# Kernel tuning notes

Measured on AMD Instinct MI355X. Metric: run time of the kernel, lower is better.

## Reference

```python
import math
import jax, jax.numpy as jnp
import numpy as np

EMB_DIM, EMB_KS, EMB_HS = 64, 2, 1
H, CS = 4, 32  # n_heads, GLA chunk size
EPS = 1e-5


def _ln4d(x, g, b):
    # LayerNormalization4D: normalize over channel dim (axis 1), biased var
    mu = x.mean(1, keepdims=True)
    var = ((x - mu) ** 2).mean(1, keepdims=True)
    return (x - mu) / jnp.sqrt(var + EPS) * g + b


def _unfold(x):
    # x [N,C,Q] -> [N, L, C*ks]; torch F.unfold feature order is c-major, k-minor
    N, C, Q = x.shape
    L = (Q - EMB_KS) // EMB_HS + 1
    f = jnp.stack([x[:, :, k:k + L] for k in range(EMB_KS)], axis=2)  # [N,C,ks,L]
    return f.reshape(N, C * EMB_KS, L).transpose(0, 2, 1)


def _deconv1d(x, w, b):
    # ConvTranspose1d, stride=EMB_HS=1; x [N,Cin,L], w [Cin,Cout,K]
    N, Cin, L = x.shape
    Cout, K = w.shape[1], w.shape[2]
    out_len = (L - 1) * EMB_HS + K
    y = jnp.zeros((N, Cout, out_len), x.dtype)
    for k in range(K):
        y = y.at[:, :, k:k + L].add(jnp.einsum('ncl,co->nol', x, w[:, :, k]))
    return y + b[None, :, None]


def _gla(x, Wq, Wk, Wv, Wg1, Wg2, Wr, gn, Wo):
    # chunked gated linear attention (use_gk=True, use_gv=False, swish output gate)
    N, L, D = x.shape
    Dk = Wq.shape[1] // H
    Dv = Wv.shape[1] // H
    Lp = -(-L // CS) * CS
    pad = Lp - L
    nc = Lp // CS
    q = (x @ Wq) * (Dk ** -0.5)
    k = x @ Wk
    v = x @ Wv
    gk = jax.nn.log_sigmoid((x @ Wg1) @ Wg2) / 32.0  # gate_logit_normalizer=32

    def chunk(t, dh):
        t = jnp.pad(t, ((0, 0), (0, pad), (0, 0)))
        return t.reshape(N, nc, CS, H, dh)

    q, k, gk, v = chunk(q, Dk), chunk(k, Dk), chunk(gk, Dk), chunk(v, Dv)
    gc = jnp.cumsum(gk, axis=2)                      # within-chunk log-decay [N,nc,CS,H,Dk]
    q_i = q * jnp.exp(gc)
    k_i = k * jnp.exp(-gc)
    mask = jnp.tril(jnp.ones((CS, CS), bool))
    A = jnp.einsum('ncthd,ncshd->nchts', q_i, k_i)   # intra-chunk scores
    A = jnp.where(mask[None, None, None], A, 0.0)
    o_intra = jnp.einsum('nchts,ncshd->ncthd', A, v)
    gl = gc[:, :, -1]                                 # chunk-total log decay [N,nc,H,Dk]
    k_o = k * jnp.exp(gl[:, :, None] - gc)

    def step(S, inp):
        qi, ko, vc, g = inp
        o = jnp.einsum('nthk,nhkv->nthv', qi, S)      # inter-chunk contribution
        S = S * jnp.exp(g)[..., None] + jnp.einsum('nthk,nthv->nhkv', ko, vc)
        return S, o

    S0 = jnp.zeros((N, H, Dk, Dv), x.dtype)
    xs = tuple(jnp.moveaxis(t, 1, 0) for t in (q_i, k_o, v, gl))
    _, o_inter = jax.lax.scan(step, S0, xs)
    o = (o_intra + jnp.moveaxis(o_inter, 0, 1)).reshape(N, Lp, H, Dv)[:, :L]
    # per-head RMSNorm + swish output gate
    o = o / jnp.sqrt(jnp.mean(o * o, -1, keepdims=True) + EPS) * gn.reshape(H, Dv)
    r = x @ Wr
    o = o.reshape(N, L, H * Dv) * (r * jax.nn.sigmoid(r))
    return o @ Wo


def _forward(x, mouth, intra_gamma, intra_beta, intra_Wq, intra_Wk, intra_Wv,
             intra_Wg1, intra_Wg2, intra_Wr, intra_gn, intra_Wo, intra_ct_w, intra_ct_b,
             inter_gamma, inter_beta, inter_Wq, inter_Wk, inter_Wv,
             inter_Wg1, inter_Wg2, inter_Wr, inter_gn, inter_Wo, inter_ct_w, inter_ct_b):
    B, C, old_T, old_Q = x.shape
    T = math.ceil((old_T - EMB_KS) / EMB_HS) * EMB_HS + EMB_KS
    Q = math.ceil((old_Q - EMB_KS) / EMB_HS) * EMB_HS + EMB_KS
    x = jnp.pad(x, ((0, 0), (0, 0), (0, T - old_T), (0, Q - old_Q)))
    # intra (frequency) path
    u = _ln4d(x, intra_gamma, intra_beta)
    u = u.transpose(0, 2, 1, 3).reshape(B * T, C, Q)
    f = _unfold(u)                                    # [B*T, Q-1, C*ks]
    g = _gla(f, intra_Wq, intra_Wk, intra_Wv, intra_Wg1, intra_Wg2, intra_Wr, intra_gn, intra_Wo)
    y = _deconv1d(g.transpose(0, 2, 1), intra_ct_w, intra_ct_b)  # [B*T, C, Q]
    y = y.reshape(B, T, C, Q).transpose(0, 2, 1, 3) + x
    # inter (time) path
    u = _ln4d(y, inter_gamma, inter_beta)
    u = u.transpose(0, 3, 1, 2).reshape(B * Q, C, T)
    f = _unfold(u)                                    # [B*Q, T-1, C*ks]
    g = _gla(f, inter_Wq, inter_Wk, inter_Wv, inter_Wg1, inter_Wg2, inter_Wr, inter_gn, inter_Wo)
    z = _deconv1d(g.transpose(0, 2, 1), inter_ct_w, inter_ct_b)  # [B*Q, C, T]
    z = z.reshape(B, Q, C, T).transpose(0, 2, 3, 1) + y
    return z[..., :old_T, :old_Q]


def setup_inputs() -> dict:
    key = jax.random.key(0)
    ks = jax.random.split(key, 32)
    D = EMB_DIM * EMB_KS       # 128 = GLA d_model
    DKV = 2 * D                # 256 (expand_k = expand_v = 2)

    def w(i, shape, fan):
        return jax.random.normal(ks[i], shape, jnp.float32) / np.sqrt(fan).astype(np.float32)

    inp = {
        'x': jax.random.normal(ks[0], (4, EMB_DIM, 256, 128), jnp.float32),
        'mouth': jax.random.normal(ks[1], (4, 1, 64, 64), jnp.float32),
    }
    for p, base in (('intra', 2), ('inter', 14)):
        inp[p + '_gamma'] = jnp.ones((1, EMB_DIM, 1, 1), jnp.float32)
        inp[p + '_beta'] = jnp.zeros((1, EMB_DIM, 1, 1), jnp.float32)
        inp[p + '_Wq'] = w(base, (D, DKV), D)
        inp[p + '_Wk'] = w(base + 1, (D, DKV), D)
        inp[p + '_Wv'] = w(base + 2, (D, DKV), D)
        inp[p + '_Wg1'] = w(base + 3, (D, 32), D)
        inp[p + '_Wg2'] = w(base + 4, (32, DKV), 32)
        inp[p + '_Wr'] = w(base + 5, (D, DKV), D)
        inp[p + '_gn'] = jnp.ones((DKV,), jnp.float32)
        inp[p + '_Wo'] = w(base + 6, (DKV, D), DKV)
        inp[p + '_ct_w'] = w(base + 7, (D, EMB_DIM, EMB_KS), D * EMB_KS)
        inp[p + '_ct_b'] = jnp.zeros((EMB_DIM,), jnp.float32)
    return inp


def reference(x, mouth, intra_gamma, intra_beta, intra_Wq, intra_Wk, intra_Wv,
              intra_Wg1, intra_Wg2, intra_Wr, intra_gn, intra_Wo, intra_ct_w, intra_ct_b,
              inter_gamma, inter_beta, inter_Wq, inter_Wk, inter_Wv,
              inter_Wg1, inter_Wg2, inter_Wr, inter_gn, inter_Wo, inter_ct_w, inter_ct_b):
    return _forward(x, mouth, intra_gamma, intra_beta, intra_Wq, intra_Wk, intra_Wv,
                    intra_Wg1, intra_Wg2, intra_Wr, intra_gn, intra_Wo, intra_ct_w, intra_ct_b,
                    inter_gamma, inter_beta, inter_Wq, inter_Wk, inter_Wv,
                    inter_Wg1, inter_Wg2, inter_Wr, inter_gn, inter_Wo, inter_ct_w, inter_ct_b)
```

## Files before the change

kernel.cpp:

```cpp
#include <hip/hip_runtime.h>

#define EPS 1e-5f

__device__ __forceinline__ float logsig(float z) {
    return fminf(z, 0.0f) - log1pf(__expf(-fabsf(z)));
}

template<int SLEN, int PSTRIDE>
__global__ __launch_bounds__(512)
__attribute__((amdgpu_waves_per_eu(2, 2)))
void gla_pass(const float* __restrict__ src, float* __restrict__ out,
              const float* __restrict__ gamma, const float* __restrict__ beta,
              const float* __restrict__ Wq, const float* __restrict__ Wk,
              const float* __restrict__ Wv, const float* __restrict__ Wg1,
              const float* __restrict__ Wg2, const float* __restrict__ Wr,
              const float* __restrict__ gn, const float* __restrict__ Wo,
              const float* __restrict__ ctw, const float* __restrict__ ctb)
{
    constexpr int NC = SLEN / 32;
    constexpr int L  = SLEN - 1;

    __shared__ __align__(16) float sxA[64][36];
    __shared__ __align__(16) float sxB[64][36];
    __shared__ __align__(16) float sxr[64][32];
    __shared__ __align__(16) float qf[32][256];
    __shared__ __align__(16) float kf[32][256];
    __shared__ __align__(16) float voc[32][256];
    __shared__ __align__(16) float uni[4608];
    __shared__ __align__(16) float fw1t[32][36];
    __shared__ __align__(16) float gprevs[128];
    __shared__ float egl[256];
    __shared__ float sgam[64], sbet[64];
    __shared__ float smu[33], sinv[33];
    __shared__ float gcarry[256];

    float* const Ats  = uni;
    float* const gdec = uni;

    const int tid  = threadIdx.x;
    const int lane = tid & 63;
    const int wv   = tid >> 6;
    const int h    = wv & 3;
    const int kh   = wv >> 2;
    const int d    = tid & 255;
    const int th   = (tid >> 8) & 1;
    const int n    = blockIdx.x;

    int b, fixedoff;
    if constexpr (PSTRIDE == 1) { b = n >> 8; fixedoff = (n & 255) * 128; }
    else                        { b = n >> 7; fixedoff = (n & 127); }
    const int cbase = (b * 64) * 32768 + fixedoff;

    if (tid < 64)  { sgam[tid] = gamma[tid]; sbet[tid] = beta[tid]; }
    if (tid < 128) gprevs[tid] = 0.0f;

    float S[32];
    #pragma unroll
    for (int k = 0; k < 32; ++k) S[k] = 0.0f;

    const float gnv  = gn[h * 64 + lane];
    const float bias = ctb[lane];

    #pragma unroll
    for (int k = 0; k < 5; ++k) {
        int idx = tid + k * 512;
        if (idx < 64 * 33) {
            int cc = idx / 33, i = idx - cc * 33;
            sxA[cc][i] = src[cbase + cc * 32768 + i * PSTRIDE];
        }
    }

    for (int ch = 0; ch < NC; ++ch) {
        const int l0 = ch * 32;
        float (* const cur)[36] = (ch & 1) ? sxB : sxA;
        float (* const nxt)[36] = (ch & 1) ? sxA : sxB;
        __syncthreads();

        float pre[5];
        const bool pf = (ch + 1 < NC);
        if (pf) {
            const int l0n = l0 + 32;
            #pragma unroll
            for (int k = 0; k < 5; ++k) {
                int idx = tid + k * 512;
                if (idx < 64 * 33) {
                    int cc = idx / 33, i = idx - cc * 33;
                    int p  = l0n + i; if (p > SLEN - 1) p = SLEN - 1;
                    pre[k] = src[cbase + cc * 32768 + p * PSTRIDE];
                }
            }
        }

        for (int col = wv; col < 33; col += 8) {
            float x = cur[lane][col];
            float s1 = x, s2 = x * x;
            #pragma unroll
            for (int off = 32; off > 0; off >>= 1) {
                s1 += __shfl_xor(s1, off, 64);
                s2 += __shfl_xor(s2, off, 64);
            }
            if (lane == 0) {
                float mu  = s1 * (1.0f / 64.0f);
                float var = s2 * (1.0f / 64.0f) - mu * mu;
                smu[col]  = mu;
                sinv[col] = rsqrtf(fmaxf(var, 0.0f) + EPS);
            }
        }
        __syncthreads();

        #pragma unroll
        for (int k = 0; k < 5; ++k) {
            int idx = tid + k * 512;
            if (idx < 64 * 33) {
                int cc = idx / 33, i = idx - cc * 33;
                float x = cur[cc][i];
                if (i < 32) sxr[cc][i] = x;
                cur[cc][i] = (x - smu[i]) * sinv[i] * sgam[cc] + sbet[cc];
            }
        }
        __syncthreads();

        {
            const int m = tid & 31, tg2 = tid >> 5;
            float a0 = 0.0f, a1 = 0.0f;
            #pragma unroll 2
            for (int cc = 0; cc < 64; ++cc) {
                const float w0 = Wg1[(2*cc)*32 + m], w1 = Wg1[(2*cc+1)*32 + m];
                a0 += cur[cc][tg2]      * w0 + cur[cc][tg2 + 1]  * w1;
                a1 += cur[cc][tg2 + 16] * w0 + cur[cc][tg2 + 17] * w1;
            }
            fw1t[m][tg2] = a0; fw1t[m][tg2 + 16] = a1;
        }
        __syncthreads();

        float rn[16];
        {
            const int t0 = th * 16;
            float acc2[16];
            #pragma unroll
            for (int t = 0; t < 16; ++t) acc2[t] = 0.0f;
            for (int mm = 0; mm < 32; ++mm) {
                const float w = Wg2[mm * 256 + d];
                #pragma unroll
                for (int i = 0; i < 4; ++i) {
                    float4 f4 = *(const float4*)&fw1t[mm][t0 + 4 * i];
                    acc2[4*i+0] += f4.x * w; acc2[4*i+1] += f4.y * w;
                    acc2[4*i+2] += f4.z * w; acc2[4*i+3] += f4.w * w;
                }
            }
            float r = 0.0f;
            #pragma unroll
            for (int t = 0; t < 16; ++t) {
                if ((l0 + t0 + t) < L) r += logsig(acc2[t]) * (1.0f / 32.0f);
                acc2[t] = r;
            }
            if (th == 0) gcarry[d] = r;
            __syncthreads();
            const float c = (th == 0) ? 0.0f : gcarry[d];
            #pragma unroll
            for (int t = 0; t < 16; ++t) rn[t] = c + acc2[t];
            if (th == 1) egl[d] = __expf(rn[15]);
        }

        if (pf) {
            #pragma unroll
            for (int k = 0; k < 5; ++k) {
                int idx = tid + k * 512;
                if (idx < 64 * 33) {
                    int cc = idx / 33, i = idx - cc * 33;
                    nxt[cc][i] = pre[k];
                }
            }
        }

        {
            const int t0 = th * 16;
            float aq[16], ak[16];
            #pragma unroll
            for (int t = 0; t < 16; ++t) { aq[t] = 0.0f; ak[t] = 0.0f; }
            for (int cc = 0; cc < 64; ++cc) {
                float col[17];
                #pragma unroll
                for (int i = 0; i < 4; ++i) {
                    float4 c4 = *(const float4*)&cur[cc][t0 + 4 * i];
                    col[4*i] = c4.x; col[4*i+1] = c4.y; col[4*i+2] = c4.z; col[4*i+3] = c4.w;
                }
                col[16] = cur[cc][t0 + 16];
                const float wq0 = Wq[(2*cc)*256 + d], wq1 = Wq[(2*cc+1)*256 + d];
                const float wk0 = Wk[(2*cc)*256 + d], wk1 = Wk[(2*cc+1)*256 + d];
                #pragma unroll
                for (int t = 0; t < 16; ++t) {
                    aq[t] += col[t] * wq0 + col[t+1] * wq1;
                    ak[t] += col[t] * wk0 + col[t+1] * wk1;
                }
            }
            #pragma unroll
            for (int t = 0; t < 16; ++t) {
                bool valid = (l0 + t0 + t) < L;
                qf[t0 + t][d] = valid ? aq[t] * 0.125f * __expf(rn[t]) : 0.0f;
                kf[t0 + t][d] = valid ? ak[t] * __expf(-rn[t]) : 0.0f;
            }
        }
        float ar[16];
        {
            const int t0 = th * 16;
            float av[16];
            #pragma unroll
            for (int t = 0; t < 16; ++t) { av[t] = 0.0f; ar[t] = 0.0f; }
            #pragma unroll 2
            for (int cc = 0; cc < 64; ++cc) {
                float col[17];
                #pragma unroll
                for (int i = 0; i < 4; ++i) {
                    float4 c4 = *(const float4*)&cur[cc][t0 + 4 * i];
                    col[4*i] = c4.x; col[4*i+1] = c4.y; col[4*i+2] = c4.z; col[4*i+3] = c4.w;
                }
                col[16] = cur[cc][t0 + 16];
                const float wv0 = Wv[(2*cc)*256 + d], wv1 = Wv[(2*cc+1)*256 + d];
                const float wr0 = Wr[(2*cc)*256 + d], wr1 = Wr[(2*cc+1)*256 + d];
                #pragma unroll
                for (int t = 0; t < 16; ++t) {
                    av[t] += col[t] * wv0 + col[t+1] * wv1;
                    ar[t] += col[t] * wr0 + col[t+1] * wr1;
                }
            }
            #pragma unroll
            for (int t = 0; t < 16; ++t)
                voc[t0 + t][d] = ((l0 + t0 + t) < L) ? av[t] : 0.0f;
        }
        __syncthreads();

        const int base = h * 64;
        float vcol[32];
        #pragma unroll
        for (int t = 0; t < 32; ++t) vcol[t] = voc[t][base + lane];

        for (int pi = lane + 64 * kh; pi < 528; pi += 128) {
            float fpi = (float)pi;
            int t = (int)((sqrtf(8.0f * fpi + 1.0f) - 1.0f) * 0.5f);
            if (((t + 1) * (t + 2)) / 2 <= pi) ++t;
            if ((t * (t + 1)) / 2 > pi) --t;
            int s = pi - (t * (t + 1)) / 2;
            float a = 0.0f;
            #pragma unroll
            for (int ii = 0; ii < 16; ++ii) {
                int i = (ii + lane) & 15;
                float4 q4 = *(const float4*)&qf[t][base + 4 * i];
                float4 k4 = *(const float4*)&kf[s][base + 4 * i];
                a += q4.x*k4.x + q4.y*k4.y + q4.z*k4.z + q4.w*k4.w;
            }
            Ats[h * 1152 + t * 36 + s] = a;
        }
        __syncthreads();

        if (kh == 1) {
            #pragma unroll
            for (int t = 0; t < 32; ++t) {
                float oe = 0.0f;
                #pragma unroll
                for (int i = 0; i < 8; ++i) {
                    float4 q4 = *(const float4*)&qf[t][base + 32 + 4 * i];
                    oe += q4.x*S[4*i] + q4.y*S[4*i+1] + q4.z*S[4*i+2] + q4.w*S[4*i+3];
                }
                voc[t][base + lane] = oe;
            }
        }
        __syncthreads();

        if (kh == 0) {
            #pragma unroll
            for (int t = 0; t < 32; ++t) {
                float ot = voc[t][base + lane];
                #pragma unroll
                for (int i = 0; i < 8; ++i) {
                    float4 q4 = *(const float4*)&qf[t][base + 4 * i];
                    ot += q4.x*S[4*i] + q4.y*S[4*i+1] + q4.z*S[4*i+2] + q4.w*S[4*i+3];
                }
                const float* arow = &Ats[h * 1152 + t * 36];
                #pragma unroll
                for (int s4 = 0; s4 + 4 <= t + 1; s4 += 4) {
                    float4 a4 = *(const float4*)&arow[s4];
                    ot += a4.x*vcol[s4] + a4.y*vcol[s4+1] + a4.z*vcol[s4+2] + a4.w*vcol[s4+3];
                }
                #pragma unroll
                for (int s = (t + 1) & ~3; s <= t; ++s) ot += arow[s] * vcol[s];
                float ss = ot * ot;
                #pragma unroll
                for (int off = 32; off > 0; off >>= 1) ss += __shfl_xor(ss, off, 64);
                voc[t][base + lane] = ot * rsqrtf(ss * (1.0f / 64.0f) + EPS) * gnv;
            }
        } else {
            const int kb = base + 32;
            #pragma unroll
            for (int i = 0; i < 8; ++i) {
                float s0 = 0.0f, s1 = 0.0f, s2 = 0.0f, s3 = 0.0f;
                #pragma unroll
                for (int t = 0; t < 32; ++t) {
                    float4 k4 = *(const float4*)&kf[t][kb + 4 * i];
                    const float vt = vcol[t];
                    s0 += k4.x * vt; s1 += k4.y * vt; s2 += k4.z * vt; s3 += k4.w * vt;
                }
                S[4*i+0] = egl[kb + 4*i+0] * (S[4*i+0] + s0);
                S[4*i+1] = egl[kb + 4*i+1] * (S[4*i+1] + s1);
                S[4*i+2] = egl[kb + 4*i+2] * (S[4*i+2] + s2);
                S[4*i+3] = egl[kb + 4*i+3] * (S[4*i+3] + s3);
            }
        }
        __syncthreads();

        if (kh == 0) {
            const int kb = base;
            #pragma unroll
            for (int i = 0; i < 8; ++i) {
                float s0 = 0.0f, s1 = 0.0f, s2 = 0.0f, s3 = 0.0f;
                #pragma unroll
                for (int t = 0; t < 32; ++t) {
                    float4 k4 = *(const float4*)&kf[t][kb + 4 * i];
                    const float vt = vcol[t];
                    s0 += k4.x * vt; s1 += k4.y * vt; s2 += k4.z * vt; s3 += k4.w * vt;
                }
                S[4*i+0] = egl[kb + 4*i+0] * (S[4*i+0] + s0);
                S[4*i+1] = egl[kb + 4*i+1] * (S[4*i+1] + s1);
                S[4*i+2] = egl[kb + 4*i+2] * (S[4*i+2] + s2);
                S[4*i+3] = egl[kb + 4*i+3] * (S[4*i+3] + s3);
            }
        }

        {
            const int t0 = th * 16;
            #pragma unroll
            for (int t = 0; t < 16; ++t) {
                const float r = ar[t];
                voc[t0 + t][d] *= r / (1.0f + __expf(-r));
            }
        }
        __syncthreads();

        {
            const int m2  = tid & 63;
            const int tg4 = tid >> 6;
            float accA[4] = {0,0,0,0}, accB[4] = {0,0,0,0};
            for (int j = 0; j < 256; j += 4) {
                float wA0 = Wo[(j+0)*128 + m2],      wB0 = Wo[(j+0)*128 + m2 + 64];
                float wA1 = Wo[(j+1)*128 + m2],      wB1 = Wo[(j+1)*128 + m2 + 64];
                float wA2 = Wo[(j+2)*128 + m2],      wB2 = Wo[(j+2)*128 + m2 + 64];
                float wA3 = Wo[(j+3)*128 + m2],      wB3 = Wo[(j+3)*128 + m2 + 64];
                #pragma unroll
                for (int i = 0; i < 4; ++i) {
                    float4 o4 = *(const float4*)&voc[tg4 * 4 + i][j];
                    accA[i] += o4.x*wA0 + o4.y*wA1 + o4.z*wA2 + o4.w*wA3;
                    accB[i] += o4.x*wB0 + o4.y*wB1 + o4.z*wB2 + o4.w*wB3;
                }
            }
            #pragma unroll
            for (int i = 0; i < 4; ++i) {
                gdec[(tg4 * 4 + i) * 132 + m2]      = accA[i];
                gdec[(tg4 * 4 + i) * 132 + m2 + 64] = accB[i];
            }
        }
        __syncthreads();

        {
            const int o  = lane;
            const int pg = wv;
            const float2* ctw2 = (const float2*)ctw;
            float acc4[4] = {0,0,0,0};
            for (int c4 = 0; c4 < 128; c4 += 4) {
                float2 w0 = ctw2[(c4+0)*64 + o];
                float2 w1 = ctw2[(c4+1)*64 + o];
                float2 w2 = ctw2[(c4+2)*64 + o];
                float2 w3 = ctw2[(c4+3)*64 + o];
                float4 r[5];
                r[0] = (pg == 0) ? *(const float4*)&gprevs[c4]
                                 : *(const float4*)&gdec[(pg*4 - 1) * 132 + c4];
                #pragma unroll
                for (int j = 0; j < 4; ++j)
                    r[j+1] = *(const float4*)&gdec[(pg*4 + j) * 132 + c4];
                #pragma unroll
                for (int i = 0; i < 4; ++i) {
                    acc4[i] += r[i+1].x*w0.x + r[i].x*w0.y
                             + r[i+1].y*w1.x + r[i].y*w1.y
                             + r[i+1].z*w2.x + r[i].z*w2.y
                             + r[i+1].w*w3.x + r[i].w*w3.y;
                }
            }
            #pragma unroll
            for (int i = 0; i < 4; ++i) {
                const int tl = pg * 4 + i;
                const int oi = cbase + o * 32768 + (l0 + tl) * PSTRIDE;
                out[oi] = acc4[i] + bias + sxr[o][tl];
            }
        }
        __syncthreads();
        if (tid < 128) gprevs[tid] = gdec[31 * 132 + tid];
    }
}

extern "C" void kernel_launch(void* const* d_in, const int* in_sizes, int n_in,
                              void* d_out, int out_size, void* d_ws, size_t ws_size,
                              hipStream_t stream)
{
    const float* x = (const float*)d_in[0];
    float* y = (float*)d_ws;
    float* z = (float*)d_out;

    gla_pass<128, 1><<<dim3(1024), dim3(512), 0, stream>>>(
        x, y,
        (const float*)d_in[2],  (const float*)d_in[3],  (const float*)d_in[4],
        (const float*)d_in[5],  (const float*)d_in[6],  (const float*)d_in[7],
        (const float*)d_in[8],  (const float*)d_in[9],  (const float*)d_in[10],
        (const float*)d_in[11], (const float*)d_in[12], (const float*)d_in[13]);

    gla_pass<256, 128><<<dim3(512), dim3(512), 0, stream>>>(
        y, z,
        (const float*)d_in[14], (const float*)d_in[15], (const float*)d_in[16],
        (const float*)d_in[17], (const float*)d_in[18], (const float*)d_in[19],
        (const float*)d_in[20], (const float*)d_in[21], (const float*)d_in[22],
        (const float*)d_in[23], (const float*)d_in[24], (const float*)d_in[25]);
}
```

Measured before the change: 6.395 ms.

## Restructure GLA pass to 256-thread blocks with per-head single-wave state

```diff
diff --git a/kernel.cpp b/kernel.cpp
--- a/kernel.cpp
+++ b/kernel.cpp
@@ -7,8 +7,7 @@
 }
 
 template<int SLEN, int PSTRIDE>
-__global__ __launch_bounds__(512)
-__attribute__((amdgpu_waves_per_eu(2, 2)))
+__global__ __launch_bounds__(256, 2)
 void gla_pass(const float* __restrict__ src, float* __restrict__ out,
               const float* __restrict__ gamma, const float* __restrict__ beta,
               const float* __restrict__ Wq, const float* __restrict__ Wk,
@@ -20,30 +19,17 @@
     constexpr int NC = SLEN / 32;
     constexpr int L  = SLEN - 1;
 
-    __shared__ __align__(16) float sxA[64][36];
-    __shared__ __align__(16) float sxB[64][36];
-    __shared__ __align__(16) float sxr[64][32];
-    __shared__ __align__(16) float qf[32][256];
-    __shared__ __align__(16) float kf[32][256];
-    __shared__ __align__(16) float voc[32][256];
-    __shared__ __align__(16) float uni[4608];
-    __shared__ __align__(16) float fw1t[32][36];
-    __shared__ __align__(16) float gprevs[128];
+    __shared__ __align__(16) float sx[64][36];
+    __shared__ __align__(16) float qfR[32 * 260];
+    __shared__ __align__(16) float kfR[32 * 260];
     __shared__ float egl[256];
+    __shared__ float gprevs[128];
     __shared__ float sgam[64], sbet[64];
-    __shared__ float smu[33], sinv[33];
-    __shared__ float gcarry[256];
-
-    float* const Ats  = uni;
-    float* const gdec = uni;
 
     const int tid  = threadIdx.x;
     const int lane = tid & 63;
-    const int wv   = tid >> 6;
-    const int h    = wv & 3;
-    const int kh   = wv >> 2;
-    const int d    = tid & 255;
-    const int th   = (tid >> 8) & 1;
+    const int h    = tid >> 6;
+    const int base = h * 64;
     const int n    = blockIdx.x;
 
     int b, fixedoff;
@@ -54,45 +40,45 @@
     if (tid < 64)  { sgam[tid] = gamma[tid]; sbet[tid] = beta[tid]; }
     if (tid < 128) gprevs[tid] = 0.0f;
 
-    float S[32];
+    float S[64];
     #pragma unroll
-    for (int k = 0; k < 32; ++k) S[k] = 0.0f;
-
-    const float gnv  = gn[h * 64 + lane];
-    const float bias = ctb[lane];
+    for (int k = 0; k < 64; ++k) S[k] = 0.0f;
+
+    const float gnv  = gn[base + lane];
+    const int   oc   = tid & 63;
+    const int   pg   = tid >> 6;
+    const float bias = ctb[oc];
 
     #pragma unroll
-    for (int k = 0; k < 5; ++k) {
-        int idx = tid + k * 512;
-        if (idx < 64 * 33) {
+    for (int k = 0; k < 9; ++k) {
+        int idx = tid + k * 256;
+        if (idx < 2112) {
             int cc = idx / 33, i = idx - cc * 33;
-            sxA[cc][i] = src[cbase + cc * 32768 + i * PSTRIDE];
+            sx[cc][i] = src[cbase + cc * 32768 + i * PSTRIDE];
         }
     }
 
     for (int ch = 0; ch < NC; ++ch) {
         const int l0 = ch * 32;
-        float (* const cur)[36] = (ch & 1) ? sxB : sxA;
-        float (* const nxt)[36] = (ch & 1) ? sxA : sxB;
-        __syncthreads();
-
-        float pre[5];
+        __syncthreads();
+
+        float pre[9];
         const bool pf = (ch + 1 < NC);
         if (pf) {
-            const int l0n = l0 + 32;
-            #pragma unroll
-            for (int k = 0; k < 5; ++k) {
-                int idx = tid + k * 512;
-                if (idx < 64 * 33) {
+            #pragma unroll
+            for (int k = 0; k < 9; ++k) {
+                int idx = tid + k * 256;
+                if (idx < 2112) {
                     int cc = idx / 33, i = idx - cc * 33;
-                    int p  = l0n + i; if (p > SLEN - 1) p = SLEN - 1;
+                    int p = l0 + 32 + i; if (p > SLEN - 1) p = SLEN - 1;
                     pre[k] = src[cbase + cc * 32768 + p * PSTRIDE];
                 }
             }
         }
 
-        for (int col = wv; col < 33; col += 8) {
-            float x = cur[lane][col];
+        if (ch > 0 && tid < 128) gprevs[tid] = kfR[31 * 260 + tid];
+        for (int col = h; col < 33; col += 4) {
+            float x = sx[lane][col];
             float s1 = x, s2 = x * x;
             #pragma unroll
             for (int off = 32; off > 0; off >>= 1) {
@@ -102,297 +88,259 @@
             if (lane == 0) {
                 float mu  = s1 * (1.0f / 64.0f);
                 float var = s2 * (1.0f / 64.0f) - mu * mu;
-                smu[col]  = mu;
-                sinv[col] = rsqrtf(fmaxf(var, 0.0f) + EPS);
-            }
-        }
-        __syncthreads();
-
-        #pragma unroll
-        for (int k = 0; k < 5; ++k) {
-            int idx = tid + k * 512;
-            if (idx < 64 * 33) {
+                qfR[col]      = mu;
+                qfR[64 + col] = rsqrtf(fmaxf(var, 0.0f) + EPS);
+            }
+        }
+        __syncthreads();
+
+        #pragma unroll
+        for (int k = 0; k < 9; ++k) {
+            int idx = tid + k * 256;
+            if (idx < 2112) {
                 int cc = idx / 33, i = idx - cc * 33;
-                float x = cur[cc][i];
-                if (i < 32) sxr[cc][i] = x;
-                cur[cc][i] = (x - smu[i]) * sinv[i] * sgam[cc] + sbet[cc];
-            }
-        }
-        __syncthreads();
-
-        {
-            const int m = tid & 31, tg2 = tid >> 5;
-            float a0 = 0.0f, a1 = 0.0f;
-            #pragma unroll 2
+                sx[cc][i] = (sx[cc][i] - qfR[i]) * qfR[64 + i] * sgam[cc] + sbet[cc];
+            }
+        }
+        __syncthreads();
+
+        {
+            const int m = tid & 31, tg = tid >> 5;
+            float a0 = 0, a1 = 0, a2 = 0, a3 = 0;
             for (int cc = 0; cc < 64; ++cc) {
-                const float w0 = Wg1[(2*cc)*32 + m], w1 = Wg1[(2*cc+1)*32 + m];
-                a0 += cur[cc][tg2]      * w0 + cur[cc][tg2 + 1]  * w1;
-                a1 += cur[cc][tg2 + 16] * w0 + cur[cc][tg2 + 17] * w1;
-            }
-            fw1t[m][tg2] = a0; fw1t[m][tg2 + 16] = a1;
-        }
-        __syncthreads();
-
-        float rn[16];
-        {
-            const int t0 = th * 16;
-            float acc2[16];
-            #pragma unroll
-            for (int t = 0; t < 16; ++t) acc2[t] = 0.0f;
+                float w0 = Wg1[(2*cc)*32 + m], w1 = Wg1[(2*cc+1)*32 + m];
+                float4 c4 = *(const float4*)&sx[cc][tg * 4];
+                float  c1 = sx[cc][tg * 4 + 4];
+                a0 += c4.x*w0 + c4.y*w1;
+                a1 += c4.y*w0 + c4.z*w1;
+                a2 += c4.z*w0 + c4.w*w1;
+                a3 += c4.w*w0 + c1  *w1;
+            }
+            kfR[m*260 + tg*4 + 0] = a0;
+            kfR[m*260 + tg*4 + 1] = a1;
+            kfR[m*260 + tg*4 + 2] = a2;
+            kfR[m*260 + tg*4 + 3] = a3;
+        }
+        __syncthreads();
+
+        float rn[32];
+        {
+            float acc[32];
+            #pragma unroll
+            for (int t = 0; t < 32; ++t) acc[t] = 0.0f;
             for (int mm = 0; mm < 32; ++mm) {
-                const float w = Wg2[mm * 256 + d];
-                #pragma unroll
-                for (int i = 0; i < 4; ++i) {
-                    float4 f4 = *(const float4*)&fw1t[mm][t0 + 4 * i];
-                    acc2[4*i+0] += f4.x * w; acc2[4*i+1] += f4.y * w;
-                    acc2[4*i+2] += f4.z * w; acc2[4*i+3] += f4.w * w;
+                float w = Wg2[mm * 256 + tid];
+                #pragma unroll
+                for (int i = 0; i < 8; ++i) {
+                    float4 f4 = *(const float4*)&kfR[mm*260 + 4*i];
+                    acc[4*i+0] += f4.x * w; acc[4*i+1] += f4.y * w;
+                    acc[4*i+2] += f4.z * w; acc[4*i+3] += f4.w * w;
                 }
             }
             float r = 0.0f;
             #pragma unroll
-            for (int t = 0; t < 16; ++t) {
-                if ((l0 + t0 + t) < L) r += logsig(acc2[t]) * (1.0f / 32.0f);
-                acc2[t] = r;
-            }
-            if (th == 0) gcarry[d] = r;
-            __syncthreads();
-            const float c = (th == 0) ? 0.0f : gcarry[d];
-            #pragma unroll
-            for (int t = 0; t < 16; ++t) rn[t] = c + acc2[t];
-            if (th == 1) egl[d] = __expf(rn[15]);
-        }
+            for (int t = 0; t < 32; ++t) {
+                if (l0 + t < L) r += logsig(acc[t]) * (1.0f / 32.0f);
+                rn[t] = r;
+            }
+            egl[tid] = __expf(rn[31]);
+        }
+        __syncthreads();
+
+
+        {
+            float aq[32];
+            #pragma unroll
+            for (int t = 0; t < 32; ++t) aq[t] = 0.0f;
+            for (int cc = 0; cc < 64; ++cc) {
+                float w0 = Wq[(2*cc)*256 + tid], w1 = Wq[(2*cc+1)*256 + tid];
+                float col[33];
+                #pragma unroll
+                for (int i = 0; i < 8; ++i) {
+                    float4 c4 = *(const float4*)&sx[cc][4*i];
+                    col[4*i]=c4.x; col[4*i+1]=c4.y; col[4*i+2]=c4.z; col[4*i+3]=c4.w;
+                }
+                col[32] = sx[cc][32];
+                #pragma unroll
+                for (int t = 0; t < 32; ++t) aq[t] += col[t]*w0 + col[t+1]*w1;
+            }
+            #pragma unroll
+            for (int t = 0; t < 32; ++t)
+                qfR[t*260 + tid] = (l0 + t < L) ? aq[t] * 0.125f * __expf(rn[t]) : 0.0f;
+        }
+        {
+            float ak[32];
+            #pragma unroll
+            for (int t = 0; t < 32; ++t) ak[t] = 0.0f;
+            for (int cc = 0; cc < 64; ++cc) {
+                float w0 = Wk[(2*cc)*256 + tid], w1 = Wk[(2*cc+1)*256 + tid];
+                float col[33];
+                #pragma unroll
+                for (int i = 0; i < 8; ++i) {
+                    float4 c4 = *(const float4*)&sx[cc][4*i];
+                    col[4*i]=c4.x; col[4*i+1]=c4.y; col[4*i+2]=c4.z; col[4*i+3]=c4.w;
+                }
+                col[32] = sx[cc][32];
+                #pragma unroll
+                for (int t = 0; t < 32; ++t) ak[t] += col[t]*w0 + col[t+1]*w1;
+            }
+            #pragma unroll
+            for (int t = 0; t < 32; ++t)
+                kfR[t*260 + tid] = (l0 + t < L) ? ak[t] * __expf(-rn[t]) : 0.0f;
+        }
+        float av[32], ar[32];
+        {
+            #pragma unroll
+            for (int t = 0; t < 32; ++t) { av[t] = 0.0f; ar[t] = 0.0f; }
+            for (int cc = 0; cc < 64; ++cc) {
+                float wv0 = Wv[(2*cc)*256 + tid], wv1 = Wv[(2*cc+1)*256 + tid];
+                float wr0 = Wr[(2*cc)*256 + tid], wr1 = Wr[(2*cc+1)*256 + tid];
+                float col[33];
+                #pragma unroll
+                for (int i = 0; i < 8; ++i) {
+                    float4 c4 = *(const float4*)&sx[cc][4*i];
+                    col[4*i]=c4.x; col[4*i+1]=c4.y; col[4*i+2]=c4.z; col[4*i+3]=c4.w;
+                }
+                col[32] = sx[cc][32];
+                #pragma unroll
+                for (int t = 0; t < 32; ++t) {
+                    av[t] += col[t]*wv0 + col[t+1]*wv1;
+                    ar[t] += col[t]*wr0 + col[t+1]*wr1;
+                }
+            }
+            #pragma unroll
+            for (int t = 0; t < 32; ++t) if (l0 + t >= L) av[t] = 0.0f;
+        }
+
+        float a[9];
+        #pragma unroll
+        for (int j = 0; j < 9; ++j) a[j] = 0.0f;
+        #pragma unroll
+        for (int j = 0; j < 9; ++j) {
+            int pi = lane + 64 * j;
+            if (pi < 528) {
+                float fpi = (float)pi;
+                int t = (int)((sqrtf(8.0f * fpi + 1.0f) - 1.0f) * 0.5f);
+                if (((t + 1) * (t + 2)) / 2 <= pi) ++t;
+                if ((t * (t + 1)) / 2 > pi) --t;
+                int s = pi - (t * (t + 1)) / 2;
+                float acc = 0.0f;
+                #pragma unroll
+                for (int ii = 0; ii < 16; ++ii) {
+                    int i = (ii + lane) & 15;
+                    float4 q4 = *(const float4*)&qfR[t*260 + base + 4*i];
+                    float4 k4 = *(const float4*)&kfR[s*260 + base + 4*i];
+                    acc += q4.x*k4.x + q4.y*k4.y + q4.z*k4.z + q4.w*k4.w;
+                }
+                a[j] = acc;
+            }
+        }
+
+        #pragma unroll
+        for (int t = 0; t < 32; ++t) {
+            float ot = 0.0f;
+            #pragma unroll
+            for (int i = 0; i < 16; ++i) {
+                float4 q4 = *(const float4*)&qfR[t*260 + base + 4*i];
+                ot += q4.x*S[4*i] + q4.y*S[4*i+1] + q4.z*S[4*i+2] + q4.w*S[4*i+3];
+            }
+            #pragma unroll
+            for (int s = 0; s <= t; ++s) {
+                const int pi = (t * (t + 1)) / 2 + s;
+                ot += __shfl(a[pi >> 6], pi & 63, 64) * av[s];
+            }
+            float ss = ot * ot;
+            #pragma unroll
+            for (int off = 32; off > 0; off >>= 1) ss += __shfl_xor(ss, off, 64);
+            qfR[t*260 + base + lane] = ot * rsqrtf(ss * (1.0f / 64.0f) + EPS) * gnv;
+        }
+
+        #pragma unroll
+        for (int i = 0; i < 16; ++i) {
+            float s0 = 0, s1 = 0, s2 = 0, s3 = 0;
+            #pragma unroll
+            for (int t = 0; t < 32; ++t) {
+                float4 k4 = *(const float4*)&kfR[t*260 + base + 4*i];
+                float vt = av[t];
+                s0 += k4.x*vt; s1 += k4.y*vt; s2 += k4.z*vt; s3 += k4.w*vt;
+            }
+            S[4*i+0] = egl[base + 4*i+0] * (S[4*i+0] + s0);
+            S[4*i+1] = egl[base + 4*i+1] * (S[4*i+1] + s1);
+            S[4*i+2] = egl[base + 4*i+2] * (S[4*i+2] + s2);
+            S[4*i+3] = egl[base + 4*i+3] * (S[4*i+3] + s3);
+        }
+
+        #pragma unroll
+        for (int t = 0; t < 32; ++t) {
+            float r = ar[t];
+            qfR[t*260 + tid] *= r / (1.0f + __expf(-r));
+        }
+        __syncthreads();
 
         if (pf) {
             #pragma unroll
-            for (int k = 0; k < 5; ++k) {
-                int idx = tid + k * 512;
-                if (idx < 64 * 33) {
+            for (int k = 0; k < 9; ++k) {
+                int idx = tid + k * 256;
+                if (idx < 2112) {
                     int cc = idx / 33, i = idx - cc * 33;
-                    nxt[cc][i] = pre[k];
-                }
-            }
-        }
-
-        {
-            const int t0 = th * 16;
-            float aq[16], ak[16];
-            #pragma unroll
-            for (int t = 0; t < 16; ++t) { aq[t] = 0.0f; ak[t] = 0.0f; }
-            for (int cc = 0; cc < 64; ++cc) {
-                float col[17];
-                #pragma unroll
-                for (int i = 0; i < 4; ++i) {
-                    float4 c4 = *(const float4*)&cur[cc][t0 + 4 * i];
-                    col[4*i] = c4.x; col[4*i+1] = c4.y; col[4*i+2] = c4.z; col[4*i+3] = c4.w;
-                }
-                col[16] = cur[cc][t0 + 16];
-                const float wq0 = Wq[(2*cc)*256 + d], wq1 = Wq[(2*cc+1)*256 + d];
-                const float wk0 = Wk[(2*cc)*256 + d], wk1 = Wk[(2*cc+1)*256 + d];
-                #pragma unroll
-                for (int t = 0; t < 16; ++t) {
-                    aq[t] += col[t] * wq0 + col[t+1] * wq1;
-                    ak[t] += col[t] * wk0 + col[t+1] * wk1;
-                }
-            }
-            #pragma unroll
-            for (int t = 0; t < 16; ++t) {
-                bool valid = (l0 + t0 + t) < L;
-                qf[t0 + t][d] = valid ? aq[t] * 0.125f * __expf(rn[t]) : 0.0f;
-                kf[t0 + t][d] = valid ? ak[t] * __expf(-rn[t]) : 0.0f;
-            }
-        }
-        float ar[16];
-        {
-            const int t0 = th * 16;
-            float av[16];
-            #pragma unroll
-            for (int t = 0; t < 16; ++t) { av[t] = 0.0f; ar[t] = 0.0f; }
-            #pragma unroll 2
-            for (int cc = 0; cc < 64; ++cc) {
-                float col[17];
-                #pragma unroll
-                for (int i = 0; i < 4; ++i) {
-                    float4 c4 = *(const float4*)&cur[cc][t0 + 4 * i];
-                    col[4*i] = c4.x; col[4*i+1] = c4.y; col[4*i+2] = c4.z; col[4*i+3] = c4.w;
-                }
-                col[16] = cur[cc][t0 + 16];
-                const float wv0 = Wv[(2*cc)*256 + d], wv1 = Wv[(2*cc+1)*256 + d];
-                const float wr0 = Wr[(2*cc)*256 + d], wr1 = Wr[(2*cc+1)*256 + d];
-                #pragma unroll
-                for (int t = 0; t < 16; ++t) {
-                    av[t] += col[t] * wv0 + col[t+1] * wv1;
-                    ar[t] += col[t] * wr0 + col[t+1] * wr1;
-                }
-            }
-            #pragma unroll
-            for (int t = 0; t < 16; ++t)
-                voc[t0 + t][d] = ((l0 + t0 + t) < L) ? av[t] : 0.0f;
-        }
-        __syncthreads();
-
-        const int base = h * 64;
-        float vcol[32];
-        #pragma unroll
-        for (int t = 0; t < 32; ++t) vcol[t] = voc[t][base + lane];
-
-        for (int pi = lane + 64 * kh; pi < 528; pi += 128) {
-            float fpi = (float)pi;
-            int t = (int)((sqrtf(8.0f * fpi + 1.0f) - 1.0f) * 0.5f);
-            if (((t + 1) * (t + 2)) / 2 <= pi) ++t;
-            if ((t * (t + 1)) / 2 > pi) --t;
-            int s = pi - (t * (t + 1)) / 2;
-            float a = 0.0f;
-            #pragma unroll
-            for (int ii = 0; ii < 16; ++ii) {
-                int i = (ii + lane) & 15;
-                float4 q4 = *(const float4*)&qf[t][base + 4 * i];
-                float4 k4 = *(const float4*)&kf[s][base + 4 * i];
-                a += q4.x*k4.x + q4.y*k4.y + q4.z*k4.z + q4.w*k4.w;
-            }
-            Ats[h * 1152 + t * 36 + s] = a;
-        }
-        __syncthreads();
-
-        if (kh == 1) {
-            #pragma unroll
-            for (int t = 0; t < 32; ++t) {
-                float oe = 0.0f;
-                #pragma unroll
-                for (int i = 0; i < 8; ++i) {
-                    float4 q4 = *(const float4*)&qf[t][base + 32 + 4 * i];
-                    oe += q4.x*S[4*i] + q4.y*S[4*i+1] + q4.z*S[4*i+2] + q4.w*S[4*i+3];
-                }
-                voc[t][base + lane] = oe;
-            }
-        }
-        __syncthreads();
-
-        if (kh == 0) {
-            #pragma unroll
-            for (int t = 0; t < 32; ++t) {
-                float ot = voc[t][base + lane];
-                #pragma unroll
-                for (int i = 0; i < 8; ++i) {
-                    float4 q4 = *(const float4*)&qf[t][base + 4 * i];
-                    ot += q4.x*S[4*i] + q4.y*S[4*i+1] + q4.z*S[4*i+2] + q4.w*S[4*i+3];
-                }
-                const float* arow = &Ats[h * 1152 + t * 36];
-                #pragma unroll
-                for (int s4 = 0; s4 + 4 <= t + 1; s4 += 4) {
-                    float4 a4 = *(const float4*)&arow[s4];
-                    ot += a4.x*vcol[s4] + a4.y*vcol[s4+1] + a4.z*vcol[s4+2] + a4.w*vcol[s4+3];
-                }
-                #pragma unroll
-                for (int s = (t + 1) & ~3; s <= t; ++s) ot += arow[s] * vcol[s];
-                float ss = ot * ot;
-                #pragma unroll
-                for (int off = 32; off > 0; off >>= 1) ss += __shfl_xor(ss, off, 64);
-                voc[t][base + lane] = ot * rsqrtf(ss * (1.0f / 64.0f) + EPS) * gnv;
-            }
-        } else {
-            const int kb = base + 32;
-            #pragma unroll
-            for (int i = 0; i < 8; ++i) {
-                float s0 = 0.0f, s1 = 0.0f, s2 = 0.0f, s3 = 0.0f;
-                #pragma unroll
-                for (int t = 0; t < 32; ++t) {
-                    float4 k4 = *(const float4*)&kf[t][kb + 4 * i];
-                    const float vt = vcol[t];
-                    s0 += k4.x * vt; s1 += k4.y * vt; s2 += k4.z * vt; s3 += k4.w * vt;
-                }
-                S[4*i+0] = egl[kb + 4*i+0] * (S[4*i+0] + s0);
-                S[4*i+1] = egl[kb + 4*i+1] * (S[4*i+1] + s1);
-                S[4*i+2] = egl[kb + 4*i+2] * (S[4*i+2] + s2);
-                S[4*i+3] = egl[kb + 4*i+3] * (S[4*i+3] + s3);
-            }
-        }
-        __syncthreads();
-
-        if (kh == 0) {
-            const int kb = base;
-            #pragma unroll
-            for (int i = 0; i < 8; ++i) {
-                float s0 = 0.0f, s1 = 0.0f, s2 = 0.0f, s3 = 0.0f;
-                #pragma unroll
-                for (int t = 0; t < 32; ++t) {
-                    float4 k4 = *(const float4*)&kf[t][kb + 4 * i];
-                    const float vt = vcol[t];
-                    s0 += k4.x * vt; s1 += k4.y * vt; s2 += k4.z * vt; s3 += k4.w * vt;
-                }
-                S[4*i+0] = egl[kb + 4*i+0] * (S[4*i+0] + s0);
-                S[4*i+1] = egl[kb + 4*i+1] * (S[4*i+1] + s1);
-                S[4*i+2] = egl[kb + 4*i+2] * (S[4*i+2] + s2);
-                S[4*i+3] = egl[kb + 4*i+3] * (S[4*i+3] + s3);
-            }
-        }
-
-        {
-            const int t0 = th * 16;
-            #pragma unroll
-            for (int t = 0; t < 16; ++t) {
-                const float r = ar[t];
-                voc[t0 + t][d] *= r / (1.0f + __expf(-r));
-            }
-        }
-        __syncthreads();
-
-        {
-            const int m2  = tid & 63;
-            const int tg4 = tid >> 6;
-            float accA[4] = {0,0,0,0}, accB[4] = {0,0,0,0};
-            for (int j = 0; j < 256; j += 4) {
-                float wA0 = Wo[(j+0)*128 + m2],      wB0 = Wo[(j+0)*128 + m2 + 64];
-                float wA1 = Wo[(j+1)*128 + m2],      wB1 = Wo[(j+1)*128 + m2 + 64];
-                float wA2 = Wo[(j+2)*128 + m2],      wB2 = Wo[(j+2)*128 + m2 + 64];
-                float wA3 = Wo[(j+3)*128 + m2],      wB3 = Wo[(j+3)*128 + m2 + 64];
-                #pragma unroll
-                for (int i = 0; i < 4; ++i) {
-                    float4 o4 = *(const float4*)&voc[tg4 * 4 + i][j];
-                    accA[i] += o4.x*wA0 + o4.y*wA1 + o4.z*wA2 + o4.w*wA3;
-                    accB[i] += o4.x*wB0 + o4.y*wB1 + o4.z*wB2 + o4.w*wB3;
-                }
-            }
-            #pragma unroll
-            for (int i = 0; i < 4; ++i) {
-                gdec[(tg4 * 4 + i) * 132 + m2]      = accA[i];
-                gdec[(tg4 * 4 + i) * 132 + m2 + 64] = accB[i];
-            }
-        }
-        __syncthreads();
-
-        {
-            const int o  = lane;
-            const int pg = wv;
+                    sx[cc][i] = pre[k];
+                }
+            }
+        }
+        float resid[8];
+        #pragma unroll
+        for (int r2 = 0; r2 < 8; ++r2)
+            resid[r2] = src[cbase + oc * 32768 + (l0 + pg * 8 + r2) * PSTRIDE];
+
+        {
+            const int m2 = tid & 127, rh = tid >> 7;
+            float acc[16];
+            #pragma unroll
+            for (int r2 = 0; r2 < 16; ++r2) acc[r2] = 0.0f;
+            for (int jb = 0; jb < 64; ++jb) {
+                float w0 = Wo[(4*jb+0)*128 + m2];
+                float w1 = Wo[(4*jb+1)*128 + m2];
+                float w2 = Wo[(4*jb+2)*128 + m2];
+                float w3 = Wo[(4*jb+3)*128 + m2];
+                #pragma unroll
+                for (int r2 = 0; r2 < 16; ++r2) {
+                    float4 o4 = *(const float4*)&qfR[(rh*16 + r2)*260 + 4*jb];
+                    acc[r2] += o4.x*w0 + o4.y*w1 + o4.z*w2 + o4.w*w3;
+                }
+            }
+            #pragma unroll
+            for (int r2 = 0; r2 < 16; ++r2)
+                kfR[(rh*16 + r2)*260 + m2] = acc[r2];
+        }
+        __syncthreads();
+
+        {
             const float2* ctw2 = (const float2*)ctw;
-            float acc4[4] = {0,0,0,0};
+            float acc8[8];
+            #pragma unroll
+            for (int r2 = 0; r2 < 8; ++r2) acc8[r2] = 0.0f;
             for (int c4 = 0; c4 < 128; c4 += 4) {
-                float2 w0 = ctw2[(c4+0)*64 + o];
-                float2 w1 = ctw2[(c4+1)*64 + o];
-                float2 w2 = ctw2[(c4+2)*64 + o];
-                float2 w3 = ctw2[(c4+3)*64 + o];
-                float4 r[5];
-                r[0] = (pg == 0) ? *(const float4*)&gprevs[c4]
-                                 : *(const float4*)&gdec[(pg*4 - 1) * 132 + c4];
-                #pragma unroll
-                for (int j = 0; j < 4; ++j)
-                    r[j+1] = *(const float4*)&gdec[(pg*4 + j) * 132 + c4];
-                #pragma unroll
-                for (int i = 0; i < 4; ++i) {
-                    acc4[i] += r[i+1].x*w0.x + r[i].x*w0.y
-                             + r[i+1].y*w1.x + r[i].y*w1.y
-                             + r[i+1].z*w2.x + r[i].z*w2.y
-                             + r[i+1].w*w3.x + r[i].w*w3.y;
-                }
-            }
-            #pragma unroll
-            for (int i = 0; i < 4; ++i) {
-                const int tl = pg * 4 + i;
-                const int oi = cbase + o * 32768 + (l0 + tl) * PSTRIDE;
-                out[oi] = acc4[i] + bias + sxr[o][tl];
-            }
-        }
-        __syncthreads();
-        if (tid < 128) gprevs[tid] = gdec[31 * 132 + tid];
+                float2 w0 = ctw2[(c4+0)*64 + oc];
+                float2 w1 = ctw2[(c4+1)*64 + oc];
+                float2 w2 = ctw2[(c4+2)*64 + oc];
+                float2 w3 = ctw2[(c4+3)*64 + oc];
+                float4 rm = (pg == 0) ? *(const float4*)&gprevs[c4]
+                                      : *(const float4*)&kfR[(pg*8 - 1)*260 + c4];
+                #pragma unroll
+                for (int r2 = 0; r2 < 8; ++r2) {
+                    float4 rr = *(const float4*)&kfR[(pg*8 + r2)*260 + c4];
+                    acc8[r2] += rr.x*w0.x + rm.x*w0.y
+                              + rr.y*w1.x + rm.y*w1.y
+                              + rr.z*w2.x + rm.z*w2.y
+                              + rr.w*w3.x + rm.w*w3.y;
+                    rm = rr;
+                }
+            }
+            #pragma unroll
+            for (int r2 = 0; r2 < 8; ++r2)
+                out[cbase + oc * 32768 + (l0 + pg * 8 + r2) * PSTRIDE]
+                    = acc8[r2] + bias + resid[r2];
+        }
     }
 }
 
@@ -404,14 +352,14 @@
     float* y = (float*)d_ws;
     float* z = (float*)d_out;
 
-    gla_pass<128, 1><<<dim3(1024), dim3(512), 0, stream>>>(
+    gla_pass<128, 1><<<dim3(1024), dim3(256), 0, stream>>>(
         x, y,
         (const float*)d_in[2],  (const float*)d_in[3],  (const float*)d_in[4],
         (const float*)d_in[5],  (const float*)d_in[6],  (const float*)d_in[7],
         (const float*)d_in[8],  (const float*)d_in[9],  (const float*)d_in[10],
         (const float*)d_in[11], (const float*)d_in[12], (const float*)d_in[13]);
 
-    gla_pass<256, 128><<<dim3(512), dim3(512), 0, stream>>>(
+    gla_pass<256, 128><<<dim3(512), dim3(256), 0, stream>>>(
         y, z,
         (const float*)d_in[14], (const float*)d_in[15], (const float*)d_in[16],
         (const float*)d_in[17], (const float*)d_in[18], (const float*)d_in[19],
```

After: 24.23 ms. +278.9%, slower.
